# Performance work log

Hardware: AMD Instinct MI355X
Metric: run time of the kernel (lower is better)

Reference implementation:

```python
import jax, jax.numpy as jnp
import numpy as np

NEG_SLOPE = 0.15


def _gcn_norm(edge_index, num_nodes):
    # PyG GCNConv default: add self-loops, symmetric normalization.
    src = jnp.concatenate([edge_index[0], jnp.arange(num_nodes)])
    dst = jnp.concatenate([edge_index[1], jnp.arange(num_nodes)])
    deg = jax.ops.segment_sum(jnp.ones_like(src, dtype=jnp.float32), dst,
                              num_segments=num_nodes)
    dis = jnp.where(deg > 0, jax.lax.rsqrt(jnp.maximum(deg, 1.0)), 0.0)
    norm = dis[src] * dis[dst]  # [E + N]
    return src, dst, norm


def _gcn_conv(h, W, b, src, dst, norm, num_nodes):
    h = h @ W                                   # dense transform first (PyG order)
    msg = h[src] * norm[:, None]                # gather + scale per edge
    out = jax.ops.segment_sum(msg, dst, num_segments=num_nodes)  # scatter-add
    return out + b


def setup_inputs() -> dict:
    key = jax.random.key(0)
    ks = jax.random.split(key, 16)
    N, E, D = 20000, 320000, 128
    x = jax.random.normal(ks[0], (N, D), dtype=jnp.float32)
    edge_index = jax.random.randint(ks[1], (2, E), 0, N, dtype=jnp.int32)
    edge_attr = jax.random.normal(ks[2], (E, 2), dtype=jnp.float32)

    def lin(k, fi, fo):
        kw, kb = jax.random.split(k)
        s = 1.0 / np.sqrt(fi)
        return (jax.random.uniform(kw, (fi, fo), jnp.float32, -s, s),
                jax.random.uniform(kb, (fo,), jnp.float32, -s, s))

    W1, b1 = lin(ks[3], D, 512)
    W2, b2 = lin(ks[4], 512, 256)
    W3, b3 = lin(ks[5], 256, 128)
    Wp, bp = lin(ks[6], 128, 16)   # pre_fc (128 -> 16)
    Wf1, bf1 = lin(ks[7], 16, 32)  # fallback MLP classifier
    Wf2, bf2 = lin(ks[8], 32, 2)
    return {"x": x, "edge_index": edge_index, "edge_attr": edge_attr,
            "W1": W1, "b1": b1, "W2": W2, "b2": b2, "W3": W3, "b3": b3,
            "Wp": Wp, "bp": bp, "Wf1": Wf1, "bf1": bf1, "Wf2": Wf2, "bf2": bf2}


def reference(x, edge_index, edge_attr, W1, b1, W2, b2, W3, b3,
              Wp, bp, Wf1, bf1, Wf2, bf2):
    N = x.shape[0]
    src, dst, norm = _gcn_norm(edge_index, N)
    lrelu = lambda h: jax.nn.leaky_relu(h, NEG_SLOPE)
    h = lrelu(_gcn_conv(x, W1, b1, src, dst, norm, N))   # dropout = identity (eval)
    h = lrelu(_gcn_conv(h, W2, b2, src, dst, norm, N))
    h = lrelu(_gcn_conv(h, W3, b3, src, dst, norm, N))
    h = h @ Wp + bp                                      # pre_fc: 128 -> 16
    h = lrelu(h @ Wf1 + bf1)                             # classifier MLP
    return h @ Wf2 + bf2                                 # [N, 2]
```

## Files before the change

kernel.cpp:

```cpp
#include <hip/hip_runtime.h>
#include <hip/hip_bf16.h>

typedef __hip_bfloat16 bf16;
typedef unsigned short ushort_t;
typedef __attribute__((ext_vector_type(8))) short short8v;
typedef __attribute__((ext_vector_type(4))) float floatx4;

#define NEG_SLOPE 0.15f

__device__ __forceinline__ float us2f(unsigned short u) {
    unsigned int x = ((unsigned int)u) << 16;
    float f;
    __builtin_memcpy(&f, &x, 4);
    return f;
}
__device__ __forceinline__ unsigned short f2us(float v) {
    bf16 h = __float2bfloat16(v);
    unsigned short u;
    __builtin_memcpy(&u, &h, 2);
    return u;
}

__global__ void detect_dtype_kernel(const unsigned int* __restrict__ xw,
                                    int* __restrict__ flag) {
    __shared__ int cnt;
    int tid = threadIdx.x;
    if (tid == 0) cnt = 0;
    __syncthreads();
    int inr = 0;
    for (int k = 0; k < 4; ++k) {
        unsigned int w = xw[tid + k * 256];
        unsigned int e = (w >> 7) & 0xFF;
        if ((w & 0xFFFF) == 0 || (e >= 100 && e <= 140)) inr++;
    }
    atomicAdd(&cnt, inr);
    __syncthreads();
    if (tid == 0) flag[0] = (cnt >= 700) ? 1 : 0;
}

__global__ void convert_x_kernel(const void* __restrict__ in, ushort_t* __restrict__ out,
                                 int n, const int* __restrict__ flag) {
    int i = blockIdx.x * blockDim.x + threadIdx.x;
    if (i >= n) return;
    out[i] = (*flag) ? ((const unsigned short*)in)[i] : f2us(((const float*)in)[i]);
}

struct PrepDesc {
    const void* src[12];
    void* dst[12];
    int n[12];
    int K[12], Nn[12];
};

__global__ void prep_small_kernel(PrepDesc d, const int* __restrict__ flag) {
    int t = blockIdx.y;
    int i = blockIdx.x * blockDim.x + threadIdx.x;
    if (i >= d.n[t]) return;
    int f = *flag;
    if (d.K[t] == 0) {
        ((float*)d.dst[t])[i] = f ? us2f(((const unsigned short*)d.src[t])[i])
                                  : ((const float*)d.src[t])[i];
    } else {
        int K = d.K[t], Nn = d.Nn[t];
        int n = i / K, k = i - n * K;
        size_t si = (size_t)k * Nn + n;
        ((ushort_t*)d.dst[t])[i] = f ? ((const unsigned short*)d.src[t])[si]
                                     : f2us(((const float*)d.src[t])[si]);
    }
}

__global__ void count_deg_kernel(const int* __restrict__ dst, int* __restrict__ deg,
                                 int E, int N) {
    int i = blockIdx.x * blockDim.x + threadIdx.x;
    if (i < E) {
        int d = dst[i];
        d = d < 0 ? 0 : (d >= N ? N - 1 : d);
        atomicAdd(&deg[d], 1);
    }
}

__global__ void scanA_kernel(const int* __restrict__ deg, int* __restrict__ incl,
                             int* __restrict__ bsum, int N) {
    __shared__ int sh[1024];
    int tid = threadIdx.x;
    int i = blockIdx.x * 1024 + tid;
    int v = (i < N) ? (deg[i] + 1) : 0;
    sh[tid] = v;
    __syncthreads();
    for (int off = 1; off < 1024; off <<= 1) {
        int t = (tid >= off) ? sh[tid - off] : 0;
        __syncthreads();
        sh[tid] += t;
        __syncthreads();
    }
    if (i < N) incl[i] = sh[tid];
    if (tid == 1023) bsum[blockIdx.x] = sh[1023];
}

__global__ void scanC_kernel(const int* __restrict__ deg, const int* __restrict__ incl,
                             const int* __restrict__ bsum, int* __restrict__ offsets,
                             int* __restrict__ cursor, float* __restrict__ dis, int N) {
    __shared__ int base_s;
    if (threadIdx.x == 0) {
        int a = 0;
        for (int b = 0; b < (int)blockIdx.x; ++b) a += bsum[b];
        base_s = a;
    }
    __syncthreads();
    int i = blockIdx.x * 1024 + threadIdx.x;
    if (i >= N) return;
    int base = base_s;
    int d = deg[i] + 1;
    int inc = incl[i];
    int excl = base + inc - d;
    offsets[i] = excl;
    cursor[i] = excl;
    dis[i] = rsqrtf((float)d);
    if (i == N - 1) offsets[N] = base + inc;
}

__global__ void fill_csr_kernel(const int* __restrict__ src, const int* __restrict__ dst,
                                const float* __restrict__ dis, int* __restrict__ cursor,
                                int2* __restrict__ edges, int E, int N, int Etot) {
    int i = blockIdx.x * blockDim.x + threadIdx.x;
    int s, d;
    if (i < E) { s = src[i]; d = dst[i]; }
    else if (i < Etot) { s = d = i - E; }
    else return;
    s = s < 0 ? 0 : (s >= N ? N - 1 : s);
    d = d < 0 ? 0 : (d >= N ? N - 1 : d);
    int pos = atomicAdd(&cursor[d], 1);
    if (pos >= 0 && pos < Etot) edges[pos] = make_int2(s, __float_as_int(dis[s]));
}

template <int VEC> struct LdT;
template <> struct LdT<2> { typedef unsigned int T; };
template <> struct LdT<4> { typedef uint2 T; };

template <int VEC>
__device__ __forceinline__ void addv(typename LdT<VEC>::T u, float w, float* acc);
template <>
__device__ __forceinline__ void addv<2>(unsigned int u, float w, float* acc) {
    acc[0] += w * us2f((unsigned short)(u & 0xFFFF));
    acc[1] += w * us2f((unsigned short)(u >> 16));
}
template <>
__device__ __forceinline__ void addv<4>(uint2 u, float w, float* acc) {
    acc[0] += w * us2f((unsigned short)(u.x & 0xFFFF));
    acc[1] += w * us2f((unsigned short)(u.x >> 16));
    acc[2] += w * us2f((unsigned short)(u.y & 0xFFFF));
    acc[3] += w * us2f((unsigned short)(u.y >> 16));
}

template <int VEC>
__global__ __launch_bounds__(256) void agg_kernel(
    const ushort_t* __restrict__ Hin, ushort_t* __restrict__ OutB,
    const int* __restrict__ offsets, const int2* __restrict__ edges,
    const float* __restrict__ dis, int N, int Etot,
    const float* __restrict__ bias, int do_lrelu) {
    typedef typename LdT<VEC>::T LT;
    const int F = VEC * 64;
    int lane = threadIdx.x & 63;
    int node = blockIdx.x * 4 + (threadIdx.x >> 6);
    if (node >= N) return;
    int beg = offsets[node], end = offsets[node + 1];
    beg = beg < 0 ? 0 : (beg > Etot ? Etot : beg);
    end = end < beg ? beg : (end > Etot ? Etot : end);

    float acc[VEC];
#pragma unroll
    for (int v = 0; v < VEC; ++v) acc[v] = 0.f;

    int fo = lane * VEC;
    int e = beg;
    for (; e + 8 <= end; e += 8) {
        int2 r[8];
#pragma unroll
        for (int j = 0; j < 8; ++j) r[j] = edges[e + j];
        LT u[8];
#pragma unroll
        for (int j = 0; j < 8; ++j) {
            int s = r[j].x;
            s = s < 0 ? 0 : (s >= N ? N - 1 : s);
            u[j] = *(const LT*)(Hin + (size_t)s * F + fo);
        }
#pragma unroll
        for (int j = 0; j < 8; ++j) addv<VEC>(u[j], __int_as_float(r[j].y), acc);
    }
    if (e + 4 <= end) {
        int2 r[4];
#pragma unroll
        for (int j = 0; j < 4; ++j) r[j] = edges[e + j];
        LT u[4];
#pragma unroll
        for (int j = 0; j < 4; ++j) {
            int s = r[j].x;
            s = s < 0 ? 0 : (s >= N ? N - 1 : s);
            u[j] = *(const LT*)(Hin + (size_t)s * F + fo);
        }
#pragma unroll
        for (int j = 0; j < 4; ++j) addv<VEC>(u[j], __int_as_float(r[j].y), acc);
        e += 4;
    }
    for (; e < end; ++e) {
        int2 r = edges[e];
        int s = r.x;
        s = s < 0 ? 0 : (s >= N ? N - 1 : s);
        LT u = *(const LT*)(Hin + (size_t)s * F + fo);
        addv<VEC>(u, __int_as_float(r.y), acc);
    }

    float dn = dis[node];
    size_t base = (size_t)node * F + fo;
    float outv[VEC];
#pragma unroll
    for (int v = 0; v < VEC; ++v) {
        float a = acc[v] * dn;
        if (bias) a += bias[fo + v];
        if (do_lrelu) a = (a > 0.f) ? a : a * NEG_SLOPE;
        outv[v] = a;
    }
    if (VEC == 2) {
        unsigned int w = ((unsigned int)f2us(outv[1]) << 16) | f2us(outv[0]);
        *(unsigned int*)(OutB + base) = w;
    } else {
        uint2 w;
        w.x = ((unsigned int)f2us(outv[1]) << 16) | f2us(outv[0]);
        w.y = ((unsigned int)f2us(outv[3]) << 16) | f2us(outv[2]);
        *(uint2*)(OutB + base) = w;
    }
}

__global__ __launch_bounds__(256) void mfma_gemm_kernel(
    const ushort_t* __restrict__ A, const ushort_t* __restrict__ Bt,
    ushort_t* __restrict__ C,
    int M, int K, int Nn, const float* __restrict__ bias, int do_lrelu) {
    __shared__ ushort_t As[128 * 40];
    __shared__ ushort_t Bs[64 * 40];

    int tid = threadIdx.x;
    int row0 = blockIdx.y * 128;
    int col0 = blockIdx.x * 64;
    int lane = tid & 63;
    int w = tid >> 6;
    int quad = lane >> 4;
    int col = lane & 15;
    int wr = (w >> 1) * 64;
    int wc = (w & 1) * 32;

    floatx4 acc[4][2];
#pragma unroll
    for (int i = 0; i < 4; ++i)
#pragma unroll
        for (int j = 0; j < 2; ++j) acc[i][j] = (floatx4){0.f, 0.f, 0.f, 0.f};

    int arow = tid >> 1;
    int aseg = (tid & 1) * 16;
    int bcol = tid >> 2;
    int bseg = (tid & 3) * 8;

    for (int k0 = 0; k0 < K; k0 += 32) {
        {
            uint4 h0 = {0, 0, 0, 0}, h1 = {0, 0, 0, 0};
            if (row0 + arow < M) {
                size_t g = (size_t)(row0 + arow) * K + k0 + aseg;
                h0 = *(const uint4*)(A + g);
                h1 = *(const uint4*)(A + g + 8);
            }
            int lb = arow * 40 + aseg;
            *(uint4*)&As[lb] = h0;
            *(uint4*)&As[lb + 8] = h1;
        }
        {
            size_t g = (size_t)(col0 + bcol) * K + k0 + bseg;
            *(uint4*)&Bs[bcol * 40 + bseg] = *(const uint4*)(Bt + g);
        }
        __syncthreads();

        short8v af[4], bf[2];
#pragma unroll
        for (int rt = 0; rt < 4; ++rt)
            af[rt] = *(const short8v*)&As[(wr + rt * 16 + col) * 40 + quad * 8];
#pragma unroll
        for (int ct = 0; ct < 2; ++ct)
            bf[ct] = *(const short8v*)&Bs[(wc + ct * 16 + col) * 40 + quad * 8];
#pragma unroll
        for (int rt = 0; rt < 4; ++rt)
#pragma unroll
            for (int ct = 0; ct < 2; ++ct)
                acc[rt][ct] = __builtin_amdgcn_mfma_f32_16x16x32_bf16(
                    af[rt], bf[ct], acc[rt][ct], 0, 0, 0);
        __syncthreads();
    }

#pragma unroll
    for (int rt = 0; rt < 4; ++rt) {
#pragma unroll
        for (int ct = 0; ct < 2; ++ct) {
            int gcol = col0 + wc + ct * 16 + col;
            float bv = bias ? bias[gcol] : 0.f;
#pragma unroll
            for (int r = 0; r < 4; ++r) {
                int grow = row0 + wr + rt * 16 + quad * 4 + r;
                if (grow >= M) continue;
                float v = acc[rt][ct][r] + bv;
                if (do_lrelu) v = (v > 0.f) ? v : v * NEG_SLOPE;
                C[(size_t)grow * Nn + gcol] = f2us(v);
            }
        }
    }
}

__global__ void head_kernel(const ushort_t* __restrict__ H,
                            const float* __restrict__ Wp, const float* __restrict__ bp,
                            const float* __restrict__ Wf1, const float* __restrict__ bf1v,
                            const float* __restrict__ Wf2, const float* __restrict__ bf2v,
                            void* __restrict__ out, int N, const int* __restrict__ flag) {
    int n = blockIdx.x * blockDim.x + threadIdx.x;
    if (n >= N) return;
    const ushort_t* h = H + (size_t)n * 128;
    float h4[16];
#pragma unroll
    for (int j = 0; j < 16; ++j) h4[j] = bp[j];
    for (int k = 0; k < 128; ++k) {
        float hv = us2f(h[k]);
#pragma unroll
        for (int j = 0; j < 16; ++j) h4[j] += hv * Wp[k * 16 + j];
    }
    float h5[32];
#pragma unroll
    for (int j = 0; j < 32; ++j) h5[j] = bf1v[j];
#pragma unroll
    for (int k = 0; k < 16; ++k) {
#pragma unroll
        for (int j = 0; j < 32; ++j) h5[j] += h4[k] * Wf1[k * 32 + j];
    }
#pragma unroll
    for (int j = 0; j < 32; ++j) h5[j] = (h5[j] > 0.f) ? h5[j] : h5[j] * NEG_SLOPE;
    float o[2];
#pragma unroll
    for (int j = 0; j < 2; ++j) {
        float a = bf2v[j];
#pragma unroll
        for (int k = 0; k < 32; ++k) a += h5[k] * Wf2[k * 2 + j];
        o[j] = a;
    }
    if (*flag) {
        ushort_t* ob = (ushort_t*)out;
        ob[(size_t)n * 2 + 0] = f2us(o[0]);
        ob[(size_t)n * 2 + 1] = f2us(o[1]);
    } else {
        float* of = (float*)out;
        of[(size_t)n * 2 + 0] = o[0];
        of[(size_t)n * 2 + 1] = o[1];
    }
}

extern "C" void kernel_launch(void* const* d_in, const int* in_sizes, int n_in,
                              void* d_out, int out_size, void* d_ws, size_t ws_size,
                              hipStream_t stream) {
    const int* ei = (const int*)d_in[1];

    const int N = in_sizes[0] / 128;
    const int E = in_sizes[1] / 2;
    const int Etot = E + N;
    const int nb = (N + 1023) / 1024;
    const int* srcv = ei;
    const int* dstv = ei + E;

    uintptr_t p = (uintptr_t)d_ws;
    auto alloc = [&](size_t bytes) -> void* {
        p = (p + 255) & ~(uintptr_t)255;
        void* r = (void*)p;
        p += bytes;
        return r;
    };
    int*      flag    = (int*)alloc(4);
    ushort_t* xb      = (ushort_t*)alloc((size_t)N * 128 * 2);
    int*      deg     = (int*)alloc((size_t)N * 4);
    int*      offsets = (int*)alloc((size_t)(N + 1) * 4);
    int*      cursor  = (int*)alloc((size_t)N * 4);
    float*    dis     = (float*)alloc((size_t)N * 4);
    int*      incl    = (int*)alloc((size_t)N * 4);
    int*      bsum    = (int*)alloc((size_t)(nb + 1) * 4);
    int2*     edges   = (int2*)alloc((size_t)Etot * 8);

    const int K1 = 128, N1 = 512, K2 = 512, N2 = 256, K3 = 256, N3 = 128;
    ushort_t* W1t = (ushort_t*)alloc((size_t)K1 * N1 * 2);
    ushort_t* W2t = (ushort_t*)alloc((size_t)K2 * N2 * 2);
    ushort_t* W3t = (ushort_t*)alloc((size_t)K3 * N3 * 2);

    float* smalls[9];
    const int wmap[9] = {4, 6, 8, 9, 10, 11, 12, 13, 14};
    for (int t = 0; t < 9; ++t)
        smalls[t] = (float*)alloc((size_t)in_sizes[wmap[t]] * 4);
    const float *b1 = smalls[0], *b2 = smalls[1], *b3 = smalls[2];
    const float *Wp = smalls[3], *bp = smalls[4];
    const float *Wf1 = smalls[5], *bf1v = smalls[6];
    const float *Wf2 = smalls[7], *bf2v = smalls[8];

    ushort_t* BufT0 = (ushort_t*)alloc((size_t)N * 128 * 2);
    char*     BufH1 = (char*)alloc((size_t)N * 512 * 2);
    ushort_t* BufT2 = (ushort_t*)alloc((size_t)N * 256 * 2);
    ushort_t* t0 = BufT0;
    ushort_t* t3 = BufT0;
    ushort_t* H1 = (ushort_t*)BufH1;
    ushort_t* H2 = (ushort_t*)BufH1;
    ushort_t* H3 = (ushort_t*)(BufH1 + (size_t)N * 256 * 2);
    ushort_t* t2 = BufT2;

    detect_dtype_kernel<<<1, 256, 0, stream>>>((const unsigned int*)d_in[0], flag);
    convert_x_kernel<<<(N * 128 + 255) / 256, 256, 0, stream>>>(d_in[0], xb, N * 128, flag);
    {
        PrepDesc pd;
        for (int t = 0; t < 9; ++t) {
            pd.src[t] = d_in[wmap[t]];
            pd.dst[t] = smalls[t];
            pd.n[t] = in_sizes[wmap[t]];
            pd.K[t] = 0; pd.Nn[t] = 0;
        }
        pd.src[9]  = d_in[3]; pd.dst[9]  = W1t; pd.n[9]  = K1 * N1; pd.K[9]  = K1; pd.Nn[9]  = N1;
        pd.src[10] = d_in[5]; pd.dst[10] = W2t; pd.n[10] = K2 * N2; pd.K[10] = K2; pd.Nn[10] = N2;
        pd.src[11] = d_in[7]; pd.dst[11] = W3t; pd.n[11] = K3 * N3; pd.K[11] = K3; pd.Nn[11] = N3;
        dim3 g((K2 * N2 + 255) / 256, 12);
        prep_small_kernel<<<g, 256, 0, stream>>>(pd, flag);
    }

    hipMemsetAsync(deg, 0, (size_t)N * 4, stream);
    count_deg_kernel<<<(E + 255) / 256, 256, 0, stream>>>(dstv, deg, E, N);
    scanA_kernel<<<nb, 1024, 0, stream>>>(deg, incl, bsum, N);
    scanC_kernel<<<nb, 1024, 0, stream>>>(deg, incl, bsum, offsets, cursor, dis, N);
    fill_csr_kernel<<<(Etot + 255) / 256, 256, 0, stream>>>(srcv, dstv, dis, cursor,
                                                            edges, E, N, Etot);

    int aggGrid = (N + 3) / 4;
    agg_kernel<2><<<aggGrid, 256, 0, stream>>>(xb, t0, offsets, edges, dis,
                                               N, Etot, nullptr, 0);
    {
        dim3 g(N1 / 64, (N + 127) / 128);
        mfma_gemm_kernel<<<g, 256, 0, stream>>>(t0, W1t, H1, N, K1, N1, b1, 1);
    }
    {
        dim3 g(N2 / 64, (N + 127) / 128);
        mfma_gemm_kernel<<<g, 256, 0, stream>>>(H1, W2t, t2, N, K2, N2, nullptr, 0);
    }
    agg_kernel<4><<<aggGrid, 256, 0, stream>>>(t2, H2, offsets, edges, dis,
                                               N, Etot, b2, 1);
    {
        dim3 g(N3 / 64, (N + 127) / 128);
        mfma_gemm_kernel<<<g, 256, 0, stream>>>(H2, W3t, t3, N, K3, N3, nullptr, 0);
    }
    agg_kernel<2><<<aggGrid, 256, 0, stream>>>(t3, H3, offsets, edges, dis,
                                               N, Etot, b3, 1);
    head_kernel<<<(N + 255) / 256, 256, 0, stream>>>(H3, Wp, bp, Wf1, bf1v, Wf2, bf2v,
                                                     d_out, N, flag);
}
```

Baseline: 274.8 us.

## Fuse last aggregation with MLP head, widen GEMM tiles, inline dtype detection

```diff
diff --git a/kernel.cpp b/kernel.cpp
--- a/kernel.cpp
+++ b/kernel.cpp
@@ -21,28 +21,25 @@
     return u;
 }
 
-__global__ void detect_dtype_kernel(const unsigned int* __restrict__ xw,
-                                    int* __restrict__ flag) {
+__device__ __forceinline__ int block_flag(const unsigned int* __restrict__ xw) {
     __shared__ int cnt;
-    int tid = threadIdx.x;
-    if (tid == 0) cnt = 0;
+    if (threadIdx.x == 0) cnt = 0;
     __syncthreads();
-    int inr = 0;
-    for (int k = 0; k < 4; ++k) {
-        unsigned int w = xw[tid + k * 256];
+    if (threadIdx.x < 256) {
+        unsigned int w = xw[threadIdx.x];
         unsigned int e = (w >> 7) & 0xFF;
-        if ((w & 0xFFFF) == 0 || (e >= 100 && e <= 140)) inr++;
-    }
-    atomicAdd(&cnt, inr);
+        if ((w & 0xFFFF) == 0 || (e >= 100 && e <= 140)) atomicAdd(&cnt, 1);
+    }
     __syncthreads();
-    if (tid == 0) flag[0] = (cnt >= 700) ? 1 : 0;
+    return cnt >= 150;
 }
 
 __global__ void convert_x_kernel(const void* __restrict__ in, ushort_t* __restrict__ out,
-                                 int n, const int* __restrict__ flag) {
+                                 int n) {
+    int f = block_flag((const unsigned int*)in);
     int i = blockIdx.x * blockDim.x + threadIdx.x;
     if (i >= n) return;
-    out[i] = (*flag) ? ((const unsigned short*)in)[i] : f2us(((const float*)in)[i]);
+    out[i] = f ? ((const unsigned short*)in)[i] : f2us(((const float*)in)[i]);
 }
 
 struct PrepDesc {
@@ -52,11 +49,11 @@
     int K[12], Nn[12];
 };
 
-__global__ void prep_small_kernel(PrepDesc d, const int* __restrict__ flag) {
+__global__ void prep_small_kernel(PrepDesc d, const void* __restrict__ xsrc) {
+    int f = block_flag((const unsigned int*)xsrc);
     int t = blockIdx.y;
     int i = blockIdx.x * blockDim.x + threadIdx.x;
     if (i >= d.n[t]) return;
-    int f = *flag;
     if (d.K[t] == 0) {
         ((float*)d.dst[t])[i] = f ? us2f(((const unsigned short*)d.src[t])[i])
                                   : ((const float*)d.src[t])[i];
@@ -153,16 +150,13 @@
 }
 
 template <int VEC>
-__global__ __launch_bounds__(256) void agg_kernel(
-    const ushort_t* __restrict__ Hin, ushort_t* __restrict__ OutB,
-    const int* __restrict__ offsets, const int2* __restrict__ edges,
-    const float* __restrict__ dis, int N, int Etot,
-    const float* __restrict__ bias, int do_lrelu) {
+__device__ __forceinline__ void agg_core(
+    const ushort_t* __restrict__ Hin, const int* __restrict__ offsets,
+    const int2* __restrict__ edges, const float* __restrict__ dis,
+    int node, int lane, int N, int Etot,
+    const float* __restrict__ bias, int do_lrelu, float* outv) {
     typedef typename LdT<VEC>::T LT;
     const int F = VEC * 64;
-    int lane = threadIdx.x & 63;
-    int node = blockIdx.x * 4 + (threadIdx.x >> 6);
-    if (node >= N) return;
     int beg = offsets[node], end = offsets[node + 1];
     beg = beg < 0 ? 0 : (beg > Etot ? Etot : beg);
     end = end < beg ? beg : (end > Etot ? Etot : end);
@@ -211,8 +205,6 @@
     }
 
     float dn = dis[node];
-    size_t base = (size_t)node * F + fo;
-    float outv[VEC];
 #pragma unroll
     for (int v = 0; v < VEC; ++v) {
         float a = acc[v] * dn;
@@ -220,6 +212,20 @@
         if (do_lrelu) a = (a > 0.f) ? a : a * NEG_SLOPE;
         outv[v] = a;
     }
+}
+
+template <int VEC>
+__global__ __launch_bounds__(256) void agg_kernel(
+    const ushort_t* __restrict__ Hin, ushort_t* __restrict__ OutB,
+    const int* __restrict__ offsets, const int2* __restrict__ edges,
+    const float* __restrict__ dis, int N, int Etot,
+    const float* __restrict__ bias, int do_lrelu) {
+    int lane = threadIdx.x & 63;
+    int node = blockIdx.x * 4 + (threadIdx.x >> 6);
+    if (node >= N) return;
+    float outv[VEC];
+    agg_core<VEC>(Hin, offsets, edges, dis, node, lane, N, Etot, bias, do_lrelu, outv);
+    size_t base = (size_t)node * (VEC * 64) + lane * VEC;
     if (VEC == 2) {
         unsigned int w = ((unsigned int)f2us(outv[1]) << 16) | f2us(outv[0]);
         *(unsigned int*)(OutB + base) = w;
@@ -231,33 +237,84 @@
     }
 }
 
-__global__ __launch_bounds__(256) void mfma_gemm_kernel(
+__global__ __launch_bounds__(256) void agg_head_kernel(
+    const ushort_t* __restrict__ Hin,
+    const int* __restrict__ offsets, const int2* __restrict__ edges,
+    const float* __restrict__ dis, int N, int Etot,
+    const float* __restrict__ b3,
+    const float* __restrict__ Wp, const float* __restrict__ bp,
+    const float* __restrict__ Wf1, const float* __restrict__ bf1v,
+    const float* __restrict__ Wf2, const float* __restrict__ bf2v,
+    void* __restrict__ out, const void* __restrict__ xsrc) {
+    int flag = block_flag((const unsigned int*)xsrc);
+    int lane = threadIdx.x & 63;
+    int node = blockIdx.x * 4 + (threadIdx.x >> 6);
+    if (node >= N) return;
+    float h[2];
+    agg_core<2>(Hin, offsets, edges, dis, node, lane, N, Etot, b3, 1, h);
+
+    int fo = lane * 2;
+    float p[16];
+#pragma unroll
+    for (int j = 0; j < 16; ++j)
+        p[j] = h[0] * Wp[fo * 16 + j] + h[1] * Wp[(fo + 1) * 16 + j];
+#pragma unroll
+    for (int m = 1; m < 64; m <<= 1) {
+#pragma unroll
+        for (int j = 0; j < 16; ++j) p[j] += __shfl_xor(p[j], m, 64);
+    }
+    float a0 = 0.f, a1 = 0.f;
+    if (lane < 32) {
+        float s = bf1v[lane];
+#pragma unroll
+        for (int k = 0; k < 16; ++k) s += (p[k] + bp[k]) * Wf1[k * 32 + lane];
+        s = (s > 0.f) ? s : s * NEG_SLOPE;
+        a0 = s * Wf2[lane * 2 + 0];
+        a1 = s * Wf2[lane * 2 + 1];
+    }
+#pragma unroll
+    for (int m = 1; m < 64; m <<= 1) {
+        a0 += __shfl_xor(a0, m, 64);
+        a1 += __shfl_xor(a1, m, 64);
+    }
+    if (lane == 0) {
+        float o0 = a0 + bf2v[0];
+        float o1 = a1 + bf2v[1];
+        if (flag) {
+            unsigned int w = ((unsigned int)f2us(o1) << 16) | f2us(o0);
+            *(unsigned int*)((ushort_t*)out + (size_t)node * 2) = w;
+        } else {
+            float2 w = make_float2(o0, o1);
+            *(float2*)((float*)out + (size_t)node * 2) = w;
+        }
+    }
+}
+
+__global__ __launch_bounds__(256) void mfma_gemm128_kernel(
     const ushort_t* __restrict__ A, const ushort_t* __restrict__ Bt,
     ushort_t* __restrict__ C,
     int M, int K, int Nn, const float* __restrict__ bias, int do_lrelu) {
     __shared__ ushort_t As[128 * 40];
-    __shared__ ushort_t Bs[64 * 40];
+    __shared__ ushort_t Bs[128 * 40];
 
     int tid = threadIdx.x;
     int row0 = blockIdx.y * 128;
-    int col0 = blockIdx.x * 64;
+    int col0 = blockIdx.x * 128;
     int lane = tid & 63;
     int w = tid >> 6;
     int quad = lane >> 4;
     int col = lane & 15;
     int wr = (w >> 1) * 64;
-    int wc = (w & 1) * 32;
-
-    floatx4 acc[4][2];
+    int wc = (w & 1) * 64;
+
+    floatx4 acc[4][4];
 #pragma unroll
     for (int i = 0; i < 4; ++i)
 #pragma unroll
-        for (int j = 0; j < 2; ++j) acc[i][j] = (floatx4){0.f, 0.f, 0.f, 0.f};
+        for (int j = 0; j < 4; ++j) acc[i][j] = (floatx4){0.f, 0.f, 0.f, 0.f};
 
     int arow = tid >> 1;
     int aseg = (tid & 1) * 16;
-    int bcol = tid >> 2;
-    int bseg = (tid & 3) * 8;
 
     for (int k0 = 0; k0 < K; k0 += 32) {
         {
@@ -272,22 +329,26 @@
             *(uint4*)&As[lb + 8] = h1;
         }
         {
-            size_t g = (size_t)(col0 + bcol) * K + k0 + bseg;
-            *(uint4*)&Bs[bcol * 40 + bseg] = *(const uint4*)(Bt + g);
+            size_t g = (size_t)(col0 + arow) * K + k0 + aseg;
+            uint4 b0 = *(const uint4*)(Bt + g);
+            uint4 b1 = *(const uint4*)(Bt + g + 8);
+            int lb = arow * 40 + aseg;
+            *(uint4*)&Bs[lb] = b0;
+            *(uint4*)&Bs[lb + 8] = b1;
         }
         __syncthreads();
 
-        short8v af[4], bf[2];
+        short8v af[4], bf[4];
 #pragma unroll
         for (int rt = 0; rt < 4; ++rt)
             af[rt] = *(const short8v*)&As[(wr + rt * 16 + col) * 40 + quad * 8];
 #pragma unroll
-        for (int ct = 0; ct < 2; ++ct)
+        for (int ct = 0; ct < 4; ++ct)
             bf[ct] = *(const short8v*)&Bs[(wc + ct * 16 + col) * 40 + quad * 8];
 #pragma unroll
         for (int rt = 0; rt < 4; ++rt)
 #pragma unroll
-            for (int ct = 0; ct < 2; ++ct)
+            for (int ct = 0; ct < 4; ++ct)
                 acc[rt][ct] = __builtin_amdgcn_mfma_f32_16x16x32_bf16(
                     af[rt], bf[ct], acc[rt][ct], 0, 0, 0);
         __syncthreads();
@@ -296,7 +357,7 @@
 #pragma unroll
     for (int rt = 0; rt < 4; ++rt) {
 #pragma unroll
-        for (int ct = 0; ct < 2; ++ct) {
+        for (int ct = 0; ct < 4; ++ct) {
             int gcol = col0 + wc + ct * 16 + col;
             float bv = bias ? bias[gcol] : 0.f;
 #pragma unroll
@@ -311,48 +372,83 @@
     }
 }
 
-__global__ void head_kernel(const ushort_t* __restrict__ H,
-                            const float* __restrict__ Wp, const float* __restrict__ bp,
-                            const float* __restrict__ Wf1, const float* __restrict__ bf1v,
-                            const float* __restrict__ Wf2, const float* __restrict__ bf2v,
-                            void* __restrict__ out, int N, const int* __restrict__ flag) {
-    int n = blockIdx.x * blockDim.x + threadIdx.x;
-    if (n >= N) return;
-    const ushort_t* h = H + (size_t)n * 128;
-    float h4[16];
-#pragma unroll
-    for (int j = 0; j < 16; ++j) h4[j] = bp[j];
-    for (int k = 0; k < 128; ++k) {
-        float hv = us2f(h[k]);
-#pragma unroll
-        for (int j = 0; j < 16; ++j) h4[j] += hv * Wp[k * 16 + j];
-    }
-    float h5[32];
-#pragma unroll
-    for (int j = 0; j < 32; ++j) h5[j] = bf1v[j];
-#pragma unroll
-    for (int k = 0; k < 16; ++k) {
-#pragma unroll
-        for (int j = 0; j < 32; ++j) h5[j] += h4[k] * Wf1[k * 32 + j];
-    }
-#pragma unroll
-    for (int j = 0; j < 32; ++j) h5[j] = (h5[j] > 0.f) ? h5[j] : h5[j] * NEG_SLOPE;
-    float o[2];
-#pragma unroll
-    for (int j = 0; j < 2; ++j) {
-        float a = bf2v[j];
-#pragma unroll
-        for (int k = 0; k < 32; ++k) a += h5[k] * Wf2[k * 2 + j];
-        o[j] = a;
-    }
-    if (*flag) {
-        ushort_t* ob = (ushort_t*)out;
-        ob[(size_t)n * 2 + 0] = f2us(o[0]);
-        ob[(size_t)n * 2 + 1] = f2us(o[1]);
-    } else {
-        float* of = (float*)out;
-        of[(size_t)n * 2 + 0] = o[0];
-        of[(size_t)n * 2 + 1] = o[1];
+__global__ __launch_bounds__(256) void mfma_gemm64_kernel(
+    const ushort_t* __restrict__ A, const ushort_t* __restrict__ Bt,
+    ushort_t* __restrict__ C,
+    int M, int K, int Nn, const float* __restrict__ bias, int do_lrelu) {
+    __shared__ ushort_t As[128 * 40];
+    __shared__ ushort_t Bs[64 * 40];
+
+    int tid = threadIdx.x;
+    int row0 = blockIdx.y * 128;
+    int col0 = blockIdx.x * 64;
+    int lane = tid & 63;
+    int w = tid >> 6;
+    int quad = lane >> 4;
+    int col = lane & 15;
+    int wr = (w >> 1) * 64;
+    int wc = (w & 1) * 32;
+
+    floatx4 acc[4][2];
+#pragma unroll
+    for (int i = 0; i < 4; ++i)
+#pragma unroll
+        for (int j = 0; j < 2; ++j) acc[i][j] = (floatx4){0.f, 0.f, 0.f, 0.f};
+
+    int arow = tid >> 1;
+    int aseg = (tid & 1) * 16;
+    int bcol = tid >> 2;
+    int bseg = (tid & 3) * 8;
+
+    for (int k0 = 0; k0 < K; k0 += 32) {
+        {
+            uint4 h0 = {0, 0, 0, 0}, h1 = {0, 0, 0, 0};
+            if (row0 + arow < M) {
+                size_t g = (size_t)(row0 + arow) * K + k0 + aseg;
+                h0 = *(const uint4*)(A + g);
+                h1 = *(const uint4*)(A + g + 8);
+            }
+            int lb = arow * 40 + aseg;
+            *(uint4*)&As[lb] = h0;
+            *(uint4*)&As[lb + 8] = h1;
+        }
+        {
+            size_t g = (size_t)(col0 + bcol) * K + k0 + bseg;
+            *(uint4*)&Bs[bcol * 40 + bseg] = *(const uint4*)(Bt + g);
+        }
+        __syncthreads();
+
+        short8v af[4], bf[2];
+#pragma unroll
+        for (int rt = 0; rt < 4; ++rt)
+            af[rt] = *(const short8v*)&As[(wr + rt * 16 + col) * 40 + quad * 8];
+#pragma unroll
+        for (int ct = 0; ct < 2; ++ct)
+            bf[ct] = *(const short8v*)&Bs[(wc + ct * 16 + col) * 40 + quad * 8];
+#pragma unroll
+        for (int rt = 0; rt < 4; ++rt)
+#pragma unroll
+            for (int ct = 0; ct < 2; ++ct)
+                acc[rt][ct] = __builtin_amdgcn_mfma_f32_16x16x32_bf16(
+                    af[rt], bf[ct], acc[rt][ct], 0, 0, 0);
+        __syncthreads();
+    }
+
+#pragma unroll
+    for (int rt = 0; rt < 4; ++rt) {
+#pragma unroll
+        for (int ct = 0; ct < 2; ++ct) {
+            int gcol = col0 + wc + ct * 16 + col;
+            float bv = bias ? bias[gcol] : 0.f;
+#pragma unroll
+            for (int r = 0; r < 4; ++r) {
+                int grow = row0 + wr + rt * 16 + quad * 4 + r;
+                if (grow >= M) continue;
+                float v = acc[rt][ct][r] + bv;
+                if (do_lrelu) v = (v > 0.f) ? v : v * NEG_SLOPE;
+                C[(size_t)grow * Nn + gcol] = f2us(v);
+            }
+        }
     }
 }
 
@@ -375,7 +471,6 @@
         p += bytes;
         return r;
     };
-    int*      flag    = (int*)alloc(4);
     ushort_t* xb      = (ushort_t*)alloc((size_t)N * 128 * 2);
     int*      deg     = (int*)alloc((size_t)N * 4);
     int*      offsets = (int*)alloc((size_t)(N + 1) * 4);
@@ -400,17 +495,15 @@
     const float *Wf2 = smalls[7], *bf2v = smalls[8];
 
     ushort_t* BufT0 = (ushort_t*)alloc((size_t)N * 128 * 2);
-    char*     BufH1 = (char*)alloc((size_t)N * 512 * 2);
+    ushort_t* BufH1 = (ushort_t*)alloc((size_t)N * 512 * 2);
     ushort_t* BufT2 = (ushort_t*)alloc((size_t)N * 256 * 2);
     ushort_t* t0 = BufT0;
     ushort_t* t3 = BufT0;
-    ushort_t* H1 = (ushort_t*)BufH1;
-    ushort_t* H2 = (ushort_t*)BufH1;
-    ushort_t* H3 = (ushort_t*)(BufH1 + (size_t)N * 256 * 2);
+    ushort_t* H1 = BufH1;
+    ushort_t* H2 = BufH1;
     ushort_t* t2 = BufT2;
 
-    detect_dtype_kernel<<<1, 256, 0, stream>>>((const unsigned int*)d_in[0], flag);
-    convert_x_kernel<<<(N * 128 + 255) / 256, 256, 0, stream>>>(d_in[0], xb, N * 128, flag);
+    convert_x_kernel<<<(N * 128 + 255) / 256, 256, 0, stream>>>(d_in[0], xb, N * 128);
     {
         PrepDesc pd;
         for (int t = 0; t < 9; ++t) {
@@ -423,7 +516,7 @@
         pd.src[10] = d_in[5]; pd.dst[10] = W2t; pd.n[10] = K2 * N2; pd.K[10] = K2; pd.Nn[10] = N2;
         pd.src[11] = d_in[7]; pd.dst[11] = W3t; pd.n[11] = K3 * N3; pd.K[11] = K3; pd.Nn[11] = N3;
         dim3 g((K2 * N2 + 255) / 256, 12);
-        prep_small_kernel<<<g, 256, 0, stream>>>(pd, flag);
+        prep_small_kernel<<<g, 256, 0, stream>>>(pd, d_in[0]);
     }
 
     hipMemsetAsync(deg, 0, (size_t)N * 4, stream);
@@ -437,21 +530,20 @@
     agg_kernel<2><<<aggGrid, 256, 0, stream>>>(xb, t0, offsets, edges, dis,
                                                N, Etot, nullptr, 0);
     {
-        dim3 g(N1 / 64, (N + 127) / 128);
-        mfma_gemm_kernel<<<g, 256, 0, stream>>>(t0, W1t, H1, N, K1, N1, b1, 1);
+        dim3 g(N1 / 128, (N + 127) / 128);
+        mfma_gemm128_kernel<<<g, 256, 0, stream>>>(t0, W1t, H1, N, K1, N1, b1, 1);
     }
     {
-        dim3 g(N2 / 64, (N + 127) / 128);
-        mfma_gemm_kernel<<<g, 256, 0, stream>>>(H1, W2t, t2, N, K2, N2, nullptr, 0);
+        dim3 g(N2 / 128, (N + 127) / 128);
+        mfma_gemm128_kernel<<<g, 256, 0, stream>>>(H1, W2t, t2, N, K2, N2, nullptr, 0);
     }
     agg_kernel<4><<<aggGrid, 256, 0, stream>>>(t2, H2, offsets, edges, dis,
                                                N, Etot, b2, 1);
     {
         dim3 g(N3 / 64, (N + 127) / 128);
-        mfma_gemm_kernel<<<g, 256, 0, stream>>>(H2, W3t, t3, N, K3, N3, nullptr, 0);
-    }
-    agg_kernel<2><<<aggGrid, 256, 0, stream>>>(t3, H3, offsets, edges, dis,
-                                               N, Etot, b3, 1);
-    head_kernel<<<(N + 255) / 256, 256, 0, stream>>>(H3, Wp, bp, Wf1, bf1v, Wf2, bf2v,
-                                                     d_out, N, flag);
-}
+        mfma_gemm64_kernel<<<g, 256, 0, stream>>>(H2, W3t, t3, N, K3, N3, nullptr, 0);
+    }
+    agg_head_kernel<<<aggGrid, 256, 0, stream>>>(t3, offsets, edges, dis, N, Etot,
+                                                 b3, Wp, bp, Wf1, bf1v, Wf2, bf2v,
+                                                 d_out, d_in[0]);
+}
```

Measured after the change: 277.5 us. About the same (+1.0%).
